# Kernel tuning notes

Hardware: AMD Instinct MI355X
Metric: run time of the kernel (lower is better)

Reference implementation:

```python
import jax, jax.numpy as jnp
import numpy as np

N_NODES = 100000
N_EDGES = 1600000
D_IN = 128
D_HID = 128
N_LAYERS = 3


def setup_inputs() -> dict:
    key = jax.random.key(0)
    k1, k2, k3, k4 = jax.random.split(key, 4)
    x = jax.random.normal(k1, (N_NODES, D_IN), dtype=jnp.float32)
    edge_index = jax.random.randint(k2, (2, N_EDGES), 0, N_NODES, dtype=jnp.int64)
    # Glorot-ish scale for stability across 3 layers
    Ws = jax.random.normal(k3, (N_LAYERS, D_IN, D_HID), dtype=jnp.float32) * (1.0 / np.sqrt(D_IN))
    bs = jax.random.normal(k4, (N_LAYERS, D_HID), dtype=jnp.float32) * 0.01
    return {"x": x, "edge_index": edge_index, "Ws": Ws, "bs": bs}


def _gcn_conv(x, row, col, deg_inv_sqrt, W, b, n_nodes):
    # Linear transform first (PyG GCNConv), then gather-normalize-scatter.
    h = x @ W                                        # [N, D]
    norm = deg_inv_sqrt[row] * deg_inv_sqrt[col]     # [E+N] (self-loops included)
    msg = h[row] * norm[:, None]                     # gather + scale, [E+N, D]
    out = jax.ops.segment_sum(msg, col, num_segments=n_nodes)  # scatter-add
    return out + b


def reference(x, edge_index, Ws, bs):
    n = x.shape[0]
    # add self-loops once (same for every layer)
    loop = jnp.arange(n, dtype=edge_index.dtype)
    row = jnp.concatenate([edge_index[0], loop])
    col = jnp.concatenate([edge_index[1], loop])
    # symmetric normalization: deg over target nodes (incl. self-loops)
    deg = jax.ops.segment_sum(jnp.ones_like(col, dtype=x.dtype), col, num_segments=n)
    deg_inv_sqrt = jnp.where(deg > 0, jax.lax.rsqrt(jnp.maximum(deg, 1.0)), 0.0)
    h = x
    for i in range(Ws.shape[0]):
        h = jax.nn.relu(_gcn_conv(h, row, col, deg_inv_sqrt, Ws[i], bs[i], n))
    return h
```

## Files before the change

kernel.cpp:

```cpp
#include <hip/hip_runtime.h>
#include <hip/hip_bf16.h>

#define NN 100000
#define NROWS 100032
#define NE 1600000
#define DD 128
#define NBUK 196
#define F1_BLOCKS 256
#define F3_BLOCKS 256
#define NGBLK 3125

typedef unsigned short ushort_t;
typedef unsigned int uint_t;
typedef unsigned long long uint64_t_;
typedef __attribute__((ext_vector_type(8))) short bf16x8;
typedef __attribute__((ext_vector_type(4))) float f32x4;

__device__ __forceinline__ ushort_t bf16rne(float f) {
    uint_t u = __float_as_uint(f);
    u += 0x7FFF + ((u >> 16) & 1);
    return (ushort_t)(u >> 16);
}
__device__ __forceinline__ float bfLo(uint_t u) { return __uint_as_float(u << 16); }
__device__ __forceinline__ float bfHi(uint_t u) { return __uint_as_float(u & 0xFFFF0000u); }


__global__ __launch_bounds__(256) void f1_bucket_count(const int* __restrict__ col,
                                                       int* __restrict__ bukCount) {
    __shared__ int hist[NBUK];
    for (int t = threadIdx.x; t < NBUK; t += 256) hist[t] = 0;
    __syncthreads();
    const int epb = (NE + F1_BLOCKS - 1) / F1_BLOCKS;
    const int e0 = blockIdx.x * epb;
    const int e1 = min(e0 + epb, NE);
    for (int e = e0 + threadIdx.x; e < e1; e += 256)
        atomicAdd(&hist[col[e] >> 9], 1);
    __syncthreads();
    for (int t = threadIdx.x; t < NBUK; t += 256)
        if (hist[t]) atomicAdd(&bukCount[t], hist[t]);
}

__global__ void f2_bucket_scan(const int* __restrict__ bukCount,
                               int* __restrict__ bukBase,
                               int* __restrict__ bukCursor,
                               int* __restrict__ offsets) {
    __shared__ int s[256];
    const int t = threadIdx.x;
    int v = (t < NBUK) ? bukCount[t] : 0;
    s[t] = v;
    __syncthreads();
    for (int off = 1; off < 256; off <<= 1) {
        int tmp = (t >= off) ? s[t - off] : 0;
        __syncthreads();
        s[t] += tmp;
        __syncthreads();
    }
    int excl = s[t] - v;
    if (t < NBUK) { bukBase[t] = excl; bukCursor[t] = excl; }
    if (t == 255) { bukBase[NBUK] = s[255]; offsets[NN] = s[255]; }
}

__global__ __launch_bounds__(256) void f3_scatter(const int* __restrict__ row,
                                                  const int* __restrict__ col,
                                                  int* __restrict__ bukCursor,
                                                  int* __restrict__ ebuf) {
    __shared__ int hist[4][NBUK];
    __shared__ int base[4][NBUK];
    const int t = threadIdx.x;
    const int w = t >> 6;
    const int lane = t & 63;
    for (int i = t; i < 4 * NBUK; i += 256) (&hist[0][0])[i] = 0;
    __syncthreads();
    const int epb = (NE + F3_BLOCKS - 1) / F3_BLOCKS;
    const int e0 = blockIdx.x * epb;
    const int e1 = min(e0 + epb, NE);
    const int wepb = (e1 - e0 + 3) >> 2;
    const int we0 = e0 + w * wepb;
    const int we1 = min(we0 + wepb, e1);
    for (int e = we0 + lane; e < we1; e += 64)
        atomicAdd(&hist[w][col[e] >> 9], 1);
    __syncthreads();
    if (t < NBUK) {
        int h0 = hist[0][t], h1 = hist[1][t], h2 = hist[2][t], h3 = hist[3][t];
        int tot = h0 + h1 + h2 + h3;
        int g = tot ? atomicAdd(&bukCursor[t], tot) : 0;
        base[0][t] = g; base[1][t] = g + h0;
        base[2][t] = g + h0 + h1; base[3][t] = g + h0 + h1 + h2;
        hist[0][t] = 0; hist[1][t] = 0; hist[2][t] = 0; hist[3][t] = 0;
    }
    __syncthreads();
    for (int e = we0 + lane; e < we1; e += 64) {
        int c = col[e];
        int b = c >> 9;
        int r = atomicAdd(&hist[w][b], 1);
        ebuf[base[w][b] + r] = (row[e] << 9) | (c & 511);
    }
}

__global__ __launch_bounds__(256) void f4_finalize(const int* __restrict__ ebuf,
                                                   const int* __restrict__ bukBase,
                                                   int* __restrict__ offsets,
                                                   float* __restrict__ dis,
                                                   int* __restrict__ csr_src) {
    __shared__ int cnt[512];
    __shared__ int cur[512];
    __shared__ int s[256];
    const int t = threadIdx.x;
    const int colBase = blockIdx.x << 9;
    const int ncols = min(512, NN - colBase);
    cnt[t] = 0; cnt[t + 256] = 0;
    __syncthreads();
    const int eb0 = bukBase[blockIdx.x];
    const int eb1 = bukBase[blockIdx.x + 1];
    for (int e = eb0 + t; e < eb1; e += 256)
        atomicAdd(&cnt[ebuf[e] & 511], 1);
    __syncthreads();
    const int c0 = cnt[2 * t], c1 = cnt[2 * t + 1];
    const int psum = c0 + c1;
    s[t] = psum;
    __syncthreads();
    for (int off = 1; off < 256; off <<= 1) {
        int tmp = (t >= off) ? s[t - off] : 0;
        __syncthreads();
        s[t] += tmp;
        __syncthreads();
    }
    const int exclPair = s[t] - psum;
    const int g0 = eb0 + exclPair;
    const int g1 = g0 + c0;
    cur[2 * t] = g0; cur[2 * t + 1] = g1;
    if (2 * t < ncols)     { offsets[colBase + 2 * t]     = g0; dis[colBase + 2 * t]     = rsqrtf((float)(c0 + 1)); }
    if (2 * t + 1 < ncols) { offsets[colBase + 2 * t + 1] = g1; dis[colBase + 2 * t + 1] = rsqrtf((float)(c1 + 1)); }
    __syncthreads();
    for (int e = eb0 + t; e < eb1; e += 256) {
        int pc = ebuf[e];
        int p = atomicAdd(&cur[pc & 511], 1);
        csr_src[p] = pc >> 9;
    }
}


__global__ __launch_bounds__(256) void wt_kernel(const float* __restrict__ Ws,
                                                 ushort_t* __restrict__ wT) {
    int idx = blockIdx.x * 256 + threadIdx.x;
    if (idx >= 3 * 128 * 16) return;
    int l = idx >> 11;
    int r = idx & 2047;
    int c = r >> 4;
    int kc = r & 15;
    const float* w = Ws + l * 16384;
    ushort_t tmp[8];
#pragma unroll
    for (int e = 0; e < 8; ++e)
        tmp[e] = bf16rne(w[(kc * 8 + e) * 128 + c]);
    *(uint4*)&wT[(size_t)l * 16384 + c * 128 + kc * 8] = *(uint4*)tmp;
}


template<bool XF32>
__global__ __launch_bounds__(256) void gemm_mfma(const void* __restrict__ Xv,
                                                 const ushort_t* __restrict__ wT,
                                                 const float* __restrict__ dis,
                                                 ushort_t* __restrict__ Y) {
    __shared__ short smem[128 * 136];
    {
        const uint4* src = (const uint4*)wT;
        int t = threadIdx.x;
#pragma unroll
        for (int i = 0; i < 8; ++i) {
            int idx = i * 256 + t;
            int rowc = idx >> 4;
            int kc = idx & 15;
            uint4 v = src[idx];
            *(uint4*)&smem[rowc * 136 + kc * 8] = v;
        }
    }
    __syncthreads();

    const int wave = threadIdx.x >> 6;
    const int lane = threadIdx.x & 63;
    const int m = lane & 15;
    const int kg = lane >> 4;
    const int r0 = blockIdx.x * 64 + wave * 16;
    const int rowA = min(r0 + m, NN - 1);

    f32x4 acc[8];
#pragma unroll
    for (int ct = 0; ct < 8; ++ct) acc[ct] = (f32x4){0.f, 0.f, 0.f, 0.f};

#pragma unroll
    for (int ks = 0; ks < 4; ++ks) {
        bf16x8 af;
        if (XF32) {
            const float* xp = (const float*)Xv + (size_t)rowA * DD + ks * 32 + kg * 8;
            float4 f0 = *(const float4*)xp;
            float4 f1 = *(const float4*)(xp + 4);
            af[0] = (short)bf16rne(f0.x); af[1] = (short)bf16rne(f0.y);
            af[2] = (short)bf16rne(f0.z); af[3] = (short)bf16rne(f0.w);
            af[4] = (short)bf16rne(f1.x); af[5] = (short)bf16rne(f1.y);
            af[6] = (short)bf16rne(f1.z); af[7] = (short)bf16rne(f1.w);
        } else {
            const ushort_t* xp = (const ushort_t*)Xv + (size_t)rowA * DD + ks * 32 + kg * 8;
            af = *(const bf16x8*)xp;
        }
#pragma unroll
        for (int ct = 0; ct < 8; ++ct) {
            bf16x8 bf = *(const bf16x8*)&smem[(ct * 16 + m) * 136 + ks * 32 + kg * 8];
            acc[ct] = __builtin_amdgcn_mfma_f32_16x16x32_bf16(af, bf, acc[ct], 0, 0, 0);
        }
    }

    __syncthreads();

    ushort_t* sl = (ushort_t*)smem;
    const int rbase = r0 + kg * 4;
    float dv[4];
#pragma unroll
    for (int rg = 0; rg < 4; ++rg) dv[rg] = dis[min(rbase + rg, NN - 1)];
#pragma unroll
    for (int ct = 0; ct < 8; ++ct) {
#pragma unroll
        for (int rg = 0; rg < 4; ++rg)
            sl[(wave * 16 + kg * 4 + rg) * 132 + ct * 16 + m] = bf16rne(acc[ct][rg] * dv[rg]);
    }

    const int i = threadIdx.x >> 2;
    const int q = threadIdx.x & 3;
    const int grow = blockIdx.x * 64 + i;
    const bool ok = grow < NN;
    const ushort_t* rb = sl + i * 132;
#pragma unroll
    for (int s = 0; s < 4; ++s) {
        const uint_t* p = (const uint_t*)(rb + s * 32 + q * 8);
        uint64_t_ d0 = (uint64_t_)p[0] | ((uint64_t_)p[1] << 32);
        uint64_t_ d1 = (uint64_t_)p[2] | ((uint64_t_)p[3] << 32);
        if (!ok) { d0 = 0ull; d1 = 0ull; }
        uint64_t_* dst = (uint64_t_*)((char*)Y + ((size_t)s * NROWS + grow) * 64 + q * 16);
        __builtin_nontemporal_store(d0, dst);
        __builtin_nontemporal_store(d1, dst + 1);
    }
}


template<bool F32OUT>
__global__ __launch_bounds__(256) void agg_kernel(const uint_t* __restrict__ lin_sl,
                                                  const int* __restrict__ offsets,
                                                  const int* __restrict__ csr_src,
                                                  const float* __restrict__ dis,
                                                  const float* __restrict__ bias,
                                                  void* __restrict__ outv) {
    const int bid  = blockIdx.x;
    const int xcd  = bid & 7;
    const int sli  = xcd >> 1;
    const int gblk = (bid >> 3) * 2 + (xcd & 1);
    if (gblk >= NGBLK) return;
    const int w    = threadIdx.x >> 6;
    const int lane = threadIdx.x & 63;
    const int g    = lane >> 3;
    const int u    = lane & 7;
    const int v    = gblk * 32 + w * 8 + g;

    const int start = offsets[v];
    const int deg   = offsets[v + 1] - start;

    const uint_t* plane = lin_sl + (size_t)sli * (NROWS * 16);

    int iv[4];
    {
        const int* cp = csr_src + start + u;
        int i0 = cp[0];
        int i1 = cp[8];
        int i2 = cp[16];
        int i3 = cp[24];
        iv[0] = (u      < deg) ? i0 : NN;
        iv[1] = (u +  8 < deg) ? i1 : NN;
        iv[2] = (u + 16 < deg) ? i2 : NN;
        iv[3] = (u + 24 < deg) ? i3 : NN;
    }

    int wmax = deg;
    wmax = max(wmax, __shfl_xor(wmax, 8));
    wmax = max(wmax, __shfl_xor(wmax, 16));
    wmax = max(wmax, __shfl_xor(wmax, 32));

    float a0 = 0.f, a1 = 0.f, a2 = 0.f, a3 = 0.f;
    const int gbase = lane & 56;
#pragma unroll
    for (int b = 0; b < 4; ++b) {
        if (b * 8 < wmax) {
#pragma unroll
            for (int jj = 0; jj < 8; ++jj) {
                int src = __shfl(iv[b], gbase + jj);
                uint2 a = *(const uint2*)(plane + ((size_t)src << 4) + u * 2);
                a0 += bfLo(a.x); a1 += bfHi(a.x);
                a2 += bfLo(a.y); a3 += bfHi(a.y);
            }
        }
    }
    {
        uint2 a = *(const uint2*)(plane + ((size_t)v << 4) + u * 2);
        a0 += bfLo(a.x); a1 += bfHi(a.x);
        a2 += bfLo(a.y); a3 += bfHi(a.y);
    }
    if (deg > 32) {
        for (int e = start + 32; e < start + deg; ++e) {
            int src = csr_src[e];
            uint2 a = *(const uint2*)(plane + ((size_t)src << 4) + u * 2);
            a0 += bfLo(a.x); a1 += bfHi(a.x);
            a2 += bfLo(a.y); a3 += bfHi(a.y);
        }
    }

    const float dv = dis[v];
    const float4 b4 = ((const float4*)bias)[sli * 8 + u];
    float r0 = fmaxf(fmaf(dv, a0, b4.x), 0.f);
    float r1 = fmaxf(fmaf(dv, a1, b4.y), 0.f);
    float r2 = fmaxf(fmaf(dv, a2, b4.z), 0.f);
    float r3 = fmaxf(fmaf(dv, a3, b4.w), 0.f);
    if (F32OUT) {
        float* op = (float*)outv + (size_t)v * DD + sli * 32 + u * 4;
        float2 lo = make_float2(r0, r1);
        float2 hi = make_float2(r2, r3);
        __builtin_nontemporal_store(*(const uint64_t_*)&lo, (uint64_t_*)op);
        __builtin_nontemporal_store(*(const uint64_t_*)&hi, (uint64_t_*)op + 1);
    } else {
        uint_t p0 = (uint_t)bf16rne(r0) | ((uint_t)bf16rne(r1) << 16);
        uint_t p1 = (uint_t)bf16rne(r2) | ((uint_t)bf16rne(r3) << 16);
        uint64_t_ pk = (uint64_t_)p0 | ((uint64_t_)p1 << 32);
        __builtin_nontemporal_store(pk, (uint64_t_*)((uint_t*)outv + (size_t)v * 64 + sli * 16 + u * 2));
    }
}


extern "C" void kernel_launch(void* const* d_in, const int* in_sizes, int n_in,
                              void* d_out, int out_size, void* d_ws, size_t ws_size,
                              hipStream_t stream) {
    const float* x   = (const float*)d_in[0];
    const int*   ei  = (const int*)d_in[1];
    const float* Ws  = (const float*)d_in[2];
    const float* bs  = (const float*)d_in[3];

    const int* row = ei;
    const int* col = ei + NE;

    char* ws = (char*)d_ws;
    ushort_t* lin    = (ushort_t*)(ws + 0);
    int*   ebuf      = (int*)  (ws + 0);
    ushort_t* hb     = (ushort_t*)(ws + 25608192);
    float* dis       = (float*)(ws + 51208192);
    int*   offsets   = (int*)  (ws + 51608192);
    int*   csr_src   = (int*)  (ws + 52008208);
    int*   bukCount  = (int*)  (ws + 58408208);
    int*   bukBase   = (int*)  (ws + 58409008);
    int*   bukCursor = (int*)  (ws + 58409808);
    ushort_t* wT     = (ushort_t*)(ws + 58410608);

    (void)hipMemsetAsync(bukCount, 0, NBUK * sizeof(int), stream);
    f1_bucket_count<<<F1_BLOCKS, 256, 0, stream>>>(col, bukCount);
    f2_bucket_scan<<<1, 256, 0, stream>>>(bukCount, bukBase, bukCursor, offsets);
    f3_scatter<<<F3_BLOCKS, 256, 0, stream>>>(row, col, bukCursor, ebuf);
    f4_finalize<<<NBUK, 256, 0, stream>>>(ebuf, bukBase, offsets, dis, csr_src);
    wt_kernel<<<24, 256, 0, stream>>>(Ws, wT);

    const int gemmGrid = NROWS / 64;
    const int aggGrid = ((NGBLK + 1) / 2) * 8;
    gemm_mfma<true><<<gemmGrid, 256, 0, stream>>>(x, wT, dis, lin);
    agg_kernel<false><<<aggGrid, 256, 0, stream>>>((const uint_t*)lin, offsets, csr_src, dis, bs, hb);
    gemm_mfma<false><<<gemmGrid, 256, 0, stream>>>(hb, wT + 16384, dis, lin);
    agg_kernel<false><<<aggGrid, 256, 0, stream>>>((const uint_t*)lin, offsets, csr_src, dis, bs + DD, hb);
    gemm_mfma<false><<<gemmGrid, 256, 0, stream>>>(hb, wT + 32768, dis, lin);
    agg_kernel<true><<<aggGrid, 256, 0, stream>>>((const uint_t*)lin, offsets, csr_src, dis, bs + 2 * DD, d_out);
}
```

Before: 300.8 us.

## Split GEMM output into eight 16-column planes and remap aggregation blocks per plane

The GEMM epilogue now writes its bf16 output as eight column planes of 16 features (32 bytes per row) instead of four planes of 32 features. The aggregation kernel maps each block-index residue mod 8 to one plane, so each plane's gather set is a smaller slice that fits better in a per-XCD L2. Each node is now handled by 4 lanes instead of 8. This trades more redundant CSR index loads and shuffles, and smaller 32-byte gathers per edge, for better cache locality. The previous pairing of two XCDs per slice is dropped.

Result: slower. 339.0 us (+12.7%).

```diff
diff --git a/kernel.cpp b/kernel.cpp
--- a/kernel.cpp
+++ b/kernel.cpp
@@ -8,7 +8,6 @@
 #define NBUK 196
 #define F1_BLOCKS 256
 #define F3_BLOCKS 256
-#define NGBLK 3125
 
 typedef unsigned short ushort_t;
 typedef unsigned int uint_t;
@@ -229,105 +228,103 @@
     const int grow = blockIdx.x * 64 + i;
     const bool ok = grow < NN;
     const ushort_t* rb = sl + i * 132;
-#pragma unroll
-    for (int s = 0; s < 4; ++s) {
-        const uint_t* p = (const uint_t*)(rb + s * 32 + q * 8);
-        uint64_t_ d0 = (uint64_t_)p[0] | ((uint64_t_)p[1] << 32);
-        uint64_t_ d1 = (uint64_t_)p[2] | ((uint64_t_)p[3] << 32);
-        if (!ok) { d0 = 0ull; d1 = 0ull; }
-        uint64_t_* dst = (uint64_t_*)((char*)Y + ((size_t)s * NROWS + grow) * 64 + q * 16);
-        __builtin_nontemporal_store(d0, dst);
-        __builtin_nontemporal_store(d1, dst + 1);
+    uint64_t_* lp2 = (uint64_t_*)Y;
+#pragma unroll
+    for (int s = 0; s < 8; ++s) {
+        const uint_t* p = (const uint_t*)(rb + s * 16 + q * 4);
+        uint64_t_ d = (uint64_t_)p[0] | ((uint64_t_)p[1] << 32);
+        uint64_t_ z = ok ? d : 0ull;
+        __builtin_nontemporal_store(z, &lp2[((size_t)s * NROWS + grow) * 4 + q]);
     }
 }
 
 
 template<bool F32OUT>
-__global__ __launch_bounds__(256) void agg_kernel(const uint_t* __restrict__ lin_sl,
+__global__ __launch_bounds__(256) void agg_kernel(const uint_t* __restrict__ lin_planes,
                                                   const int* __restrict__ offsets,
                                                   const int* __restrict__ csr_src,
                                                   const float* __restrict__ dis,
                                                   const float* __restrict__ bias,
                                                   void* __restrict__ outv) {
     const int bid  = blockIdx.x;
-    const int xcd  = bid & 7;
-    const int sli  = xcd >> 1;
-    const int gblk = (bid >> 3) * 2 + (xcd & 1);
-    if (gblk >= NGBLK) return;
+    const int s    = bid & 7;
+    const int gblk = bid >> 3;
     const int w    = threadIdx.x >> 6;
     const int lane = threadIdx.x & 63;
-    const int g    = lane >> 3;
-    const int u    = lane & 7;
-    const int v    = gblk * 32 + w * 8 + g;
-
-    const int start = offsets[v];
-    const int deg   = offsets[v + 1] - start;
-
-    const uint_t* plane = lin_sl + (size_t)sli * (NROWS * 16);
-
-    int iv[4];
+    const int g    = lane >> 2;
+    const int u    = lane & 3;
+    const int v    = gblk * 64 + w * 16 + g;
+    const int vv   = min(v, NN - 1);
+
+    const int start = offsets[vv];
+    const int deg   = offsets[vv + 1] - start;
+
+    const uint_t* plane = lin_planes + (size_t)s * (NROWS * 8);
+
+    int iv[8];
     {
         const int* cp = csr_src + start + u;
-        int i0 = cp[0];
-        int i1 = cp[8];
-        int i2 = cp[16];
-        int i3 = cp[24];
-        iv[0] = (u      < deg) ? i0 : NN;
-        iv[1] = (u +  8 < deg) ? i1 : NN;
-        iv[2] = (u + 16 < deg) ? i2 : NN;
-        iv[3] = (u + 24 < deg) ? i3 : NN;
+#pragma unroll
+        for (int k = 0; k < 8; ++k) {
+            int t = cp[4 * k];
+            iv[k] = (u + 4 * k < deg) ? t : NN;
+        }
     }
 
     int wmax = deg;
+    wmax = max(wmax, __shfl_xor(wmax, 4));
     wmax = max(wmax, __shfl_xor(wmax, 8));
     wmax = max(wmax, __shfl_xor(wmax, 16));
     wmax = max(wmax, __shfl_xor(wmax, 32));
 
     float a0 = 0.f, a1 = 0.f, a2 = 0.f, a3 = 0.f;
-    const int gbase = lane & 56;
+    const int gbase = lane & 60;
 #pragma unroll
     for (int b = 0; b < 4; ++b) {
         if (b * 8 < wmax) {
 #pragma unroll
             for (int jj = 0; jj < 8; ++jj) {
-                int src = __shfl(iv[b], gbase + jj);
-                uint2 a = *(const uint2*)(plane + ((size_t)src << 4) + u * 2);
+                const int j = b * 8 + jj;
+                int src = __shfl(iv[j >> 2], gbase + (j & 3));
+                uint2 a = *(const uint2*)(plane + ((size_t)src << 3) + u * 2);
                 a0 += bfLo(a.x); a1 += bfHi(a.x);
                 a2 += bfLo(a.y); a3 += bfHi(a.y);
             }
         }
     }
     {
-        uint2 a = *(const uint2*)(plane + ((size_t)v << 4) + u * 2);
+        uint2 a = *(const uint2*)(plane + ((size_t)vv << 3) + u * 2);
         a0 += bfLo(a.x); a1 += bfHi(a.x);
         a2 += bfLo(a.y); a3 += bfHi(a.y);
     }
     if (deg > 32) {
         for (int e = start + 32; e < start + deg; ++e) {
             int src = csr_src[e];
-            uint2 a = *(const uint2*)(plane + ((size_t)src << 4) + u * 2);
+            uint2 a = *(const uint2*)(plane + ((size_t)src << 3) + u * 2);
             a0 += bfLo(a.x); a1 += bfHi(a.x);
             a2 += bfLo(a.y); a3 += bfHi(a.y);
         }
     }
 
-    const float dv = dis[v];
-    const float4 b4 = ((const float4*)bias)[sli * 8 + u];
-    float r0 = fmaxf(fmaf(dv, a0, b4.x), 0.f);
-    float r1 = fmaxf(fmaf(dv, a1, b4.y), 0.f);
-    float r2 = fmaxf(fmaf(dv, a2, b4.z), 0.f);
-    float r3 = fmaxf(fmaf(dv, a3, b4.w), 0.f);
-    if (F32OUT) {
-        float* op = (float*)outv + (size_t)v * DD + sli * 32 + u * 4;
-        float2 lo = make_float2(r0, r1);
-        float2 hi = make_float2(r2, r3);
-        __builtin_nontemporal_store(*(const uint64_t_*)&lo, (uint64_t_*)op);
-        __builtin_nontemporal_store(*(const uint64_t_*)&hi, (uint64_t_*)op + 1);
-    } else {
-        uint_t p0 = (uint_t)bf16rne(r0) | ((uint_t)bf16rne(r1) << 16);
-        uint_t p1 = (uint_t)bf16rne(r2) | ((uint_t)bf16rne(r3) << 16);
-        uint64_t_ pk = (uint64_t_)p0 | ((uint64_t_)p1 << 32);
-        __builtin_nontemporal_store(pk, (uint64_t_*)((uint_t*)outv + (size_t)v * 64 + sli * 16 + u * 2));
+    if (v < NN) {
+        const float dv = dis[v];
+        const float4 b4 = ((const float4*)bias)[s * 4 + u];
+        float r0 = fmaxf(fmaf(dv, a0, b4.x), 0.f);
+        float r1 = fmaxf(fmaf(dv, a1, b4.y), 0.f);
+        float r2 = fmaxf(fmaf(dv, a2, b4.z), 0.f);
+        float r3 = fmaxf(fmaf(dv, a3, b4.w), 0.f);
+        if (F32OUT) {
+            float* op = (float*)outv + (size_t)v * DD + s * 16 + u * 4;
+            float2 lo = make_float2(r0, r1);
+            float2 hi = make_float2(r2, r3);
+            __builtin_nontemporal_store(*(const uint64_t_*)&lo, (uint64_t_*)op);
+            __builtin_nontemporal_store(*(const uint64_t_*)&hi, (uint64_t_*)op + 1);
+        } else {
+            uint_t p0 = (uint_t)bf16rne(r0) | ((uint_t)bf16rne(r1) << 16);
+            uint_t p1 = (uint_t)bf16rne(r2) | ((uint_t)bf16rne(r3) << 16);
+            uint64_t_ pk = (uint64_t_)p0 | ((uint64_t_)p1 << 32);
+            __builtin_nontemporal_store(pk, (uint64_t_*)((uint_t*)outv + (size_t)v * 64 + s * 8 + u * 2));
+        }
     }
 }
 
@@ -363,7 +360,7 @@
     wt_kernel<<<24, 256, 0, stream>>>(Ws, wT);
 
     const int gemmGrid = NROWS / 64;
-    const int aggGrid = ((NGBLK + 1) / 2) * 8;
+    const int aggGrid = (NROWS / 64) * 8;
     gemm_mfma<true><<<gemmGrid, 256, 0, stream>>>(x, wT, dis, lin);
     agg_kernel<false><<<aggGrid, 256, 0, stream>>>((const uint_t*)lin, offsets, csr_src, dis, bs, hb);
     gemm_mfma<false><<<gemmGrid, 256, 0, stream>>>(hb, wT + 16384, dis, lin);
```
